# Kernel optimization log

Measured on AMD Instinct MI355X. Metric: run time of the kernel, lower is better.

The kernel has to match this reference:

```python
import jax, jax.numpy as jnp
import numpy as np

N, E = 50000, 400000
IN_F, HID, HEADS, CLASSES, GROUP = 256, 64, 4, 40, 2
NEG_SLOPE = 0.2
EPS = 1e-5


def setup_inputs() -> dict:
    key = jax.random.key(0)
    ks = jax.random.split(key, 16)
    s = 0.05
    W = HEADS * HID          # 256 flattened hidden width
    GW = W // GROUP          # 128 per-group width
    GD = HID // GROUP        # 32  per-head out_feats in middle blocks
    x = jax.random.normal(ks[0], (N, IN_F), jnp.float32)
    src = jax.random.randint(ks[1], (E,), 0, N, dtype=jnp.int32)
    # guarantee every node has >=1 incoming edge so edge_softmax is well-defined
    dst = jnp.concatenate([jnp.arange(N, dtype=jnp.int32),
                           jax.random.randint(ks[2], (E - N,), 0, N, dtype=jnp.int32)])
    return dict(
        x=x, src=src, dst=dst,
        W0=jax.random.normal(ks[3], (W, IN_F)) * s,
        attn_l0=jax.random.normal(ks[4], (HEADS, HID)) * s,
        attn_r0=jax.random.normal(ks[5], (HEADS, HID)) * s,
        resW0=jax.random.normal(ks[6], (W, IN_F)) * s,
        mid_bn_gamma=jnp.ones((2, GROUP, GW)),
        mid_bn_beta=jnp.zeros((2, GROUP, GW)),
        mid_W=jax.random.normal(ks[7], (2, GROUP, GW, GW)) * s,
        mid_attn_l=jax.random.normal(ks[8], (2, GROUP, HEADS, GD)) * s,
        mid_attn_r=jax.random.normal(ks[9], (2, GROUP, HEADS, GD)) * s,
        mid_resW=jax.random.normal(ks[10], (2, GROUP, GW, GW)) * s,
        norm_gamma=jnp.ones((W,)), norm_beta=jnp.zeros((W,)),
        W_last=jax.random.normal(ks[11], (CLASSES, W)) * s,
        attn_l_last=jax.random.normal(ks[12], (1, CLASSES)) * s,
        attn_r_last=jax.random.normal(ks[13], (1, CLASSES)) * s,
        resW_last=jax.random.normal(ks[14], (CLASSES, W)) * s,
        bias_last=jnp.zeros((CLASSES,)),
    )


def _gat_conv(x, src, dst, W, attn_l, attn_r, resW, out_isqrt, in_sqrt):
    n = x.shape[0]
    H, D = attn_l.shape
    ft0 = (x @ W.T).reshape(n, H, D)            # projected feat [N,H,D]
    ft = ft0 * out_isqrt[:, None, None]         # symmetric norm on source side
    el = (ft * attn_l).sum(-1)                  # [N,H] (uses normalized feat_src)
    er = (ft0 * attn_r).sum(-1)                 # [N,H] (feat_dst aliased BEFORE norm)
    e = el[src] + er[dst]                       # edge scores [E,H]
    e = jnp.where(e >= 0, e, NEG_SLOPE * e)     # leaky_relu
    emax = jax.ops.segment_max(e, dst, num_segments=n)
    emax = jnp.where(jnp.isfinite(emax), emax, 0.0)
    ex = jnp.exp(e - emax[dst])
    denom = jax.ops.segment_sum(ex, dst, num_segments=n)
    a = ex / jnp.maximum(denom, 1e-9)[dst]      # per-destination edge softmax [E,H]
    msg = ft[src] * a[:, :, None]               # [E,H,D]
    rst = jax.ops.segment_sum(msg, dst, num_segments=n)
    rst = rst * in_sqrt[:, None, None]          # symmetric norm on dest side
    rst = rst + (x @ resW.T).reshape(n, H, D)   # residual fc
    return rst


def _bn_relu(z, gamma, beta):
    mu = z.mean(0)
    var = ((z - mu) ** 2).mean(0)               # biased var (torch BN training)
    return jax.nn.relu(gamma * (z - mu) * jax.lax.rsqrt(var + EPS) + beta)


def reference(x, src, dst, W0, attn_l0, attn_r0, resW0, mid_bn_gamma, mid_bn_beta,
              mid_W, mid_attn_l, mid_attn_r, mid_resW, norm_gamma, norm_beta,
              W_last, attn_l_last, attn_r_last, resW_last, bias_last):
    n = x.shape[0]
    ones = jnp.ones((src.shape[0],), x.dtype)
    outdeg = jnp.maximum(jax.ops.segment_sum(ones, src, num_segments=n), 1.0)
    indeg = jnp.maximum(jax.ops.segment_sum(ones, dst, num_segments=n), 1.0)
    out_isqrt = outdeg ** -0.5
    in_sqrt = jnp.sqrt(indeg)
    # layer 0: GATConv(in_feats -> n_hidden, n_heads)
    h = _gat_conv(x, src, dst, W0, attn_l0, attn_r0, resW0, out_isqrt, in_sqrt).reshape(n, -1)
    # reversible middle layers: GroupAdditiveCoupling, group=2
    for l in range(2):
        x0, x1 = jnp.split(h, 2, axis=-1)
        z = _bn_relu(x1, mid_bn_gamma[l, 0], mid_bn_beta[l, 0])
        y0 = x0 + _gat_conv(z, src, dst, mid_W[l, 0], mid_attn_l[l, 0], mid_attn_r[l, 0],
                            mid_resW[l, 0], out_isqrt, in_sqrt).reshape(n, -1)
        z = _bn_relu(y0, mid_bn_gamma[l, 1], mid_bn_beta[l, 1])
        y1 = x1 + _gat_conv(z, src, dst, mid_W[l, 1], mid_attn_l[l, 1], mid_attn_r[l, 1],
                            mid_resW[l, 1], out_isqrt, in_sqrt).reshape(n, -1)
        h = jnp.concatenate([y0, y1], axis=-1)
    # final norm + relu + output conv (1 head), mean over head dim, bias_last
    h = _bn_relu(h, norm_gamma, norm_beta)
    out = _gat_conv(h, src, dst, W_last, attn_l_last, attn_r_last, resW_last,
                    out_isqrt, in_sqrt).mean(1)
    return out + bias_last
```

## Files before the change

### kernel.cpp

```cpp
#include <hip/hip_runtime.h>
#include <hip/hip_bf16.h>


#define IN_F   256
#define HIDW   256
#define CLS    40

typedef __attribute__((ext_vector_type(8))) __bf16 bf16x8;
typedef __attribute__((ext_vector_type(4))) float  f32x4;

__device__ inline bf16x8 zb8() {
    bf16x8 v;
#pragma unroll
    for (int i = 0; i < 8; ++i) v[i] = (__bf16)0.f;
    return v;
}
__device__ inline bf16x8 ldb8(const __hip_bfloat16* p) {
    return *reinterpret_cast<const bf16x8*>(p);
}
__device__ inline float bf2f(unsigned short u) {
    union { unsigned int i; float f; } c;
    c.i = ((unsigned int)u) << 16;
    return c.f;
}
__device__ inline unsigned short f2bu(float f) {
    __hip_bfloat16 t = __float2bfloat16(f);
    union { __hip_bfloat16 b; unsigned short u; } c;
    c.b = t;
    return c.u;
}

__global__ void k_hist(const int* __restrict__ src, const int* __restrict__ dst,
                       int E, int* __restrict__ outdeg, int* __restrict__ indeg) {
    for (int e = blockIdx.x * blockDim.x + threadIdx.x; e < E; e += gridDim.x * blockDim.x) {
        atomicAdd(&outdeg[src[e]], 1);
        atomicAdd(&indeg[dst[e]], 1);
    }
}

__global__ void k_scan1(const int* __restrict__ cnt, int N, int* __restrict__ rp1,
                        int* __restrict__ bsum) {
    __shared__ int sm[256];
    int i = blockIdx.x * 256 + threadIdx.x;
    int v = (i < N) ? cnt[i] : 0;
    sm[threadIdx.x] = v;
    __syncthreads();
    for (int off = 1; off < 256; off <<= 1) {
        int t = (threadIdx.x >= off) ? sm[threadIdx.x - off] : 0;
        __syncthreads();
        sm[threadIdx.x] += t;
        __syncthreads();
    }
    if (i < N) rp1[i] = sm[threadIdx.x];
    if (threadIdx.x == 255) bsum[blockIdx.x] = sm[255];
}

__global__ void k_scan2(int* __restrict__ bsum, int nb) {
    __shared__ int sm[256];
    int v = (threadIdx.x < nb) ? bsum[threadIdx.x] : 0;
    sm[threadIdx.x] = v;
    __syncthreads();
    for (int off = 1; off < 256; off <<= 1) {
        int t = (threadIdx.x >= off) ? sm[threadIdx.x - off] : 0;
        __syncthreads();
        sm[threadIdx.x] += t;
        __syncthreads();
    }
    if (threadIdx.x < nb) bsum[threadIdx.x] = sm[threadIdx.x] - v;
}

__global__ void k_scan3(int* __restrict__ rp1, const int* __restrict__ bsumExcl, int N) {
    int i = blockIdx.x * 256 + threadIdx.x;
    if (i < N) rp1[i] += bsumExcl[blockIdx.x];
    if (blockIdx.x == 0 && threadIdx.x == 0) rp1[-1] = 0;
}

__global__ void k_scatter(const int* __restrict__ src, const int* __restrict__ dst,
                          int E, int* __restrict__ cursor, int* __restrict__ csr_src) {
    for (int e = blockIdx.x * blockDim.x + threadIdx.x; e < E; e += gridDim.x * blockDim.x) {
        int d = dst[e];
        int pos = atomicAdd(&cursor[d], 1);
        csr_src[pos] = src[e];
    }
}

__global__ void k_deg(const int* __restrict__ outdeg, const int* __restrict__ indeg,
                      float* __restrict__ oi, float* __restrict__ insq, int N) {
    int i = blockIdx.x * 256 + threadIdx.x;
    if (i < N) {
        int od = outdeg[i]; if (od < 1) od = 1;
        int id = indeg[i];  if (id < 1) id = 1;
        oi[i]   = rsqrtf((float)od);
        insq[i] = sqrtf((float)id);
    }
}

__global__ void k_cvt6(const float* s0, __hip_bfloat16* d0, int n0,
                       const float* s1, __hip_bfloat16* d1, int n1,
                       const float* s2, __hip_bfloat16* d2, int n2,
                       const float* s3, __hip_bfloat16* d3, int n3,
                       const float* s4, __hip_bfloat16* d4, int n4,
                       const float* s5, __hip_bfloat16* d5, int n5) {
    const float* ss; __hip_bfloat16* dd; int nn;
    switch (blockIdx.y) {
        case 0: ss = s0; dd = d0; nn = n0; break;
        case 1: ss = s1; dd = d1; nn = n1; break;
        case 2: ss = s2; dd = d2; nn = n2; break;
        case 3: ss = s3; dd = d3; nn = n3; break;
        case 4: ss = s4; dd = d4; nn = n4; break;
        default: ss = s5; dd = d5; nn = n5; break;
    }
    for (int i = blockIdx.x * blockDim.x + threadIdx.x; i < nn; i += gridDim.x * blockDim.x)
        dd[i] = __float2bfloat16(ss[i]);
}

__global__ void k_prepw(const float* __restrict__ W0,
                        const float* __restrict__ al0, const float* __restrict__ ar0,
                        const float* __restrict__ midW,
                        const float* __restrict__ midal, const float* __restrict__ midar,
                        __hip_bfloat16* __restrict__ Waug0,
                        __hip_bfloat16* __restrict__ midWaug) {
    const int layer = blockIdx.y;
    int NF, K, D;
    const float *W, *al, *ar;
    __hip_bfloat16* dst;
    if (layer == 0) {
        NF = 256; K = 256; D = 64;
        W = W0; al = al0; ar = ar0; dst = Waug0;
    } else {
        const int pg = layer - 1;
        NF = 128; K = 128; D = 32;
        W = midW + pg * 16384; al = midal + pg * 128; ar = midar + pg * 128;
        dst = midWaug + (size_t)pg * 144 * 128;
    }
    const int total = (NF + 16) * K;
    for (int idx = blockIdx.x * 256 + threadIdx.x; idx < total; idx += gridDim.x * 256) {
        const int col = idx / K, k = idx % K;
        float v = 0.f;
        if (col < NF) {
            v = W[(size_t)col * K + k];
        } else {
            const int j = col - NF;
            if (j < 8) {
                const int head = j & 3;
                const float* at = (j < 4) ? al : ar;
                float s = 0.f;
                for (int d = 0; d < D; ++d)
                    s += W[(size_t)(head * D + d) * K + k] * at[head * D + d];
                v = s;
            }
        }
        dst[idx] = __float2bfloat16(v);
    }
}

template<int K, int NF, int NR, int H, bool BN>
__global__ __launch_bounds__(512) void k_gatconv_lds(
    const float* __restrict__ A, int lda,
    const __hip_bfloat16* __restrict__ Waug,
    const __hip_bfloat16* __restrict__ Wres,
    __hip_bfloat16* __restrict__ ftb, int ldft,
    float* __restrict__ Cres, int ldcres, int M,
    const float* __restrict__ scale, const float* __restrict__ shift,
    const float* __restrict__ resbase, int ldbase,
    const float* __restrict__ oi,
    float* __restrict__ el, float* __restrict__ er) {
    constexpr int BM = 32, KF = K / 32, NTOT = NF + NR;
    constexpr int CW = NTOT / 8, CT = CW / 16;
    static_assert(NTOT % 8 == 0 && CW % 16 == 0, "col split");
    static_assert(NF % CW == 0, "ft/res wave boundary");
    static_assert(H == 4, "el/er float4 stores assume H==4");
    __shared__ bf16x8 lds[2 * KF * 64];
    const int tid = threadIdx.x;
    const int wv = tid >> 6, lane = tid & 63, rf = lane & 15, kg = lane >> 4;
    const int row0 = blockIdx.x * BM;

    {
        constexpr int CPR = K / 8;
        constexpr int RSTEP = 512 / CPR;
        const int c16 = tid % CPR;
        const int ec = c16 * 8;
        const int skf = c16 >> 2, skg = c16 & 3;
        float sc[8], sh[8];
        if (BN) {
            float4 s01 = *reinterpret_cast<const float4*>(scale + ec);
            float4 s23 = *reinterpret_cast<const float4*>(scale + ec + 4);
            float4 h01 = *reinterpret_cast<const float4*>(shift + ec);
            float4 h23 = *reinterpret_cast<const float4*>(shift + ec + 4);
            sc[0]=s01.x; sc[1]=s01.y; sc[2]=s01.z; sc[3]=s01.w;
            sc[4]=s23.x; sc[5]=s23.y; sc[6]=s23.z; sc[7]=s23.w;
            sh[0]=h01.x; sh[1]=h01.y; sh[2]=h01.z; sh[3]=h01.w;
            sh[4]=h23.x; sh[5]=h23.y; sh[6]=h23.z; sh[7]=h23.w;
        }
#pragma unroll
        for (int r0 = 0; r0 < BM; r0 += RSTEP) {
            const int r = r0 + tid / CPR;
            if (r < BM) {
                const int gr = row0 + r;
                bf16x8 t = zb8();
                if (gr < M) {
                    const float* ap = A + (size_t)gr * lda + ec;
                    float4 f0 = *reinterpret_cast<const float4*>(ap);
                    float4 f1 = *reinterpret_cast<const float4*>(ap + 4);
                    float v[8] = {f0.x, f0.y, f0.z, f0.w, f1.x, f1.y, f1.z, f1.w};
#pragma unroll
                    for (int i = 0; i < 8; ++i) {
                        float u = v[i];
                        if (BN) u = fmaxf(u * sc[i] + sh[i], 0.f);
                        t[i] = (__bf16)u;
                    }
                }
                lds[((r >> 4) * KF + skf) * 64 + ((skg * 16 + (r & 15)) ^ skf)] = t;
            }
        }
    }
    __syncthreads();

    const bool isft = (wv * CW) < NF;
    const int colbase = isft ? wv * CW : wv * CW - NF;
    const __hip_bfloat16* __restrict__ Wb = isft ? Waug : Wres;

    bf16x8 a0[KF], a1[KF];
#pragma unroll
    for (int kf = 0; kf < KF; ++kf) {
        a0[kf] = lds[(0 * KF + kf) * 64 + (lane ^ kf)];
        a1[kf] = lds[(1 * KF + kf) * 64 + (lane ^ kf)];
    }
    const int r0g = row0 + rf;
    const int r1g = r0g + 16;

    for (int ct = 0; ct < CT; ++ct) {
        const int tcol = colbase + ct * 16;
        bf16x8 w[KF];
        const __hip_bfloat16* bp = Wb + (size_t)(tcol + rf) * K + kg * 8;
#pragma unroll
        for (int kf = 0; kf < KF; ++kf) w[kf] = ldb8(bp + kf * 32);
        f32x4 acc0 = {0.f, 0.f, 0.f, 0.f};
        f32x4 acc1 = {0.f, 0.f, 0.f, 0.f};
#pragma unroll
        for (int kf = 0; kf < KF; ++kf) {
            acc0 = __builtin_amdgcn_mfma_f32_16x16x32_bf16(w[kf], a0[kf], acc0, 0, 0, 0);
            acc1 = __builtin_amdgcn_mfma_f32_16x16x32_bf16(w[kf], a1[kf], acc1, 0, 0, 0);
        }
        const int c4 = tcol + 4 * kg;
        if (isft) {
            if (r0g < M) {
                ushort4 q = {f2bu(acc0[0]), f2bu(acc0[1]), f2bu(acc0[2]), f2bu(acc0[3])};
                *reinterpret_cast<ushort4*>(&ftb[(size_t)r0g * ldft + c4]) = q;
            }
            if (r1g < M) {
                ushort4 q = {f2bu(acc1[0]), f2bu(acc1[1]), f2bu(acc1[2]), f2bu(acc1[3])};
                *reinterpret_cast<ushort4*>(&ftb[(size_t)r1g * ldft + c4]) = q;
            }
        } else {
            if (r0g < M) {
                float4 v = {acc0[0], acc0[1], acc0[2], acc0[3]};
                if (resbase) {
                    float4 b4 = *reinterpret_cast<const float4*>(
                        &resbase[(size_t)r0g * ldbase + c4]);
                    v.x += b4.x; v.y += b4.y; v.z += b4.z; v.w += b4.w;
                }
                *reinterpret_cast<float4*>(&Cres[(size_t)r0g * ldcres + c4]) = v;
            }
            if (r1g < M) {
                float4 v = {acc1[0], acc1[1], acc1[2], acc1[3]};
                if (resbase) {
                    float4 b4 = *reinterpret_cast<const float4*>(
                        &resbase[(size_t)r1g * ldbase + c4]);
                    v.x += b4.x; v.y += b4.y; v.z += b4.z; v.w += b4.w;
                }
                *reinterpret_cast<float4*>(&Cres[(size_t)r1g * ldcres + c4]) = v;
            }
        }
    }

    if (wv == 0) {
        bf16x8 w[KF];
        const __hip_bfloat16* bp = Waug + (size_t)(NF + rf) * K + kg * 8;
#pragma unroll
        for (int kf = 0; kf < KF; ++kf) w[kf] = ldb8(bp + kf * 32);
        f32x4 acc0 = {0.f, 0.f, 0.f, 0.f};
        f32x4 acc1 = {0.f, 0.f, 0.f, 0.f};
#pragma unroll
        for (int kf = 0; kf < KF; ++kf) {
            acc0 = __builtin_amdgcn_mfma_f32_16x16x32_bf16(w[kf], a0[kf], acc0, 0, 0, 0);
            acc1 = __builtin_amdgcn_mfma_f32_16x16x32_bf16(w[kf], a1[kf], acc1, 0, 0, 0);
        }
        if (kg == 0) {
            if (r0g < M) {
                const float o = oi[r0g];
                float4 v = {acc0[0] * o, acc0[1] * o, acc0[2] * o, acc0[3] * o};
                *reinterpret_cast<float4*>(&el[(size_t)r0g * 4]) = v;
            }
            if (r1g < M) {
                const float o = oi[r1g];
                float4 v = {acc1[0] * o, acc1[1] * o, acc1[2] * o, acc1[3] * o};
                *reinterpret_cast<float4*>(&el[(size_t)r1g * 4]) = v;
            }
        } else if (kg == 1) {
            if (r0g < M) {
                float4 v = {acc0[0], acc0[1], acc0[2], acc0[3]};
                *reinterpret_cast<float4*>(&er[(size_t)r0g * 4]) = v;
            }
            if (r1g < M) {
                float4 v = {acc1[0], acc1[1], acc1[2], acc1[3]};
                *reinterpret_cast<float4*>(&er[(size_t)r1g * 4]) = v;
            }
        }
    }
}

template<int K, int NF, int NR, int H, bool BN>
__global__ __launch_bounds__(256) void k_gatconv_sm(
    const float* __restrict__ A, int lda,
    const __hip_bfloat16* __restrict__ Wft,
    const __hip_bfloat16* __restrict__ Wres,
    __hip_bfloat16* __restrict__ ftb, int ldft,
    float* __restrict__ Cres, int ldcres,
    int M,
    const float* __restrict__ scale, const float* __restrict__ shift,
    const float* __restrict__ resbase, int ldbase,
    const float* __restrict__ bias,
    const float* __restrict__ attn_l, const float* __restrict__ attn_r,
    const float* __restrict__ oi,
    float* __restrict__ el, float* __restrict__ er) {
    constexpr int KF   = K / 32;
    constexpr int NCTF = (NF + 15) / 16;
    constexpr int NCTR = (NR + 15) / 16;
    constexpr int CTH  = NCTF / H;
    static_assert(NCTF % H == 0, "head tiling");
    const int wave = threadIdx.x >> 6, lane = threadIdx.x & 63;
    const int row0 = blockIdx.x * 64 + wave * 16;
    const int rf = lane & 15, kg = lane >> 4;

    bf16x8 a[KF];
    {
        const int row = row0 + rf;
        const bool rok = row < M;
#pragma unroll
        for (int kf = 0; kf < KF; ++kf) {
            const int c0 = kg * 8 + kf * 32;
            if (rok) {
                const float* ap = A + (size_t)row * lda + c0;
                float4 f0 = *reinterpret_cast<const float4*>(ap);
                float4 f1 = *reinterpret_cast<const float4*>(ap + 4);
                float v[8] = {f0.x, f0.y, f0.z, f0.w, f1.x, f1.y, f1.z, f1.w};
                bf16x8 t;
                if (BN) {
                    float4 s01 = *reinterpret_cast<const float4*>(scale + c0);
                    float4 s23 = *reinterpret_cast<const float4*>(scale + c0 + 4);
                    float4 h01 = *reinterpret_cast<const float4*>(shift + c0);
                    float4 h23 = *reinterpret_cast<const float4*>(shift + c0 + 4);
                    float sc[8] = {s01.x,s01.y,s01.z,s01.w,s23.x,s23.y,s23.z,s23.w};
                    float sh[8] = {h01.x,h01.y,h01.z,h01.w,h23.x,h23.y,h23.z,h23.w};
#pragma unroll
                    for (int i = 0; i < 8; ++i)
                        t[i] = (__bf16)fmaxf(v[i] * sc[i] + sh[i], 0.f);
                } else {
#pragma unroll
                    for (int i = 0; i < 8; ++i) t[i] = (__bf16)v[i];
                }
                a[kf] = t;
            } else {
                a[kf] = zb8();
            }
        }
    }

    int ct = 0;
    for (int hh = 0; hh < H; ++hh) {
        float elp[4] = {0.f, 0.f, 0.f, 0.f};
        float erp[4] = {0.f, 0.f, 0.f, 0.f};
        for (int cth = 0; cth < CTH; ++cth, ++ct) {
            const int ccol = ct * 16 + rf;
            bf16x8 b[KF];
            const __hip_bfloat16* bp = Wft + (size_t)ccol * K + kg * 8;
#pragma unroll
            for (int kf = 0; kf < KF; ++kf)
                b[kf] = (ccol < NF) ? ldb8(bp + kf * 32) : zb8();
            f32x4 acc = {0.f, 0.f, 0.f, 0.f};
#pragma unroll
            for (int kf = 0; kf < KF; ++kf)
                acc = __builtin_amdgcn_mfma_f32_16x16x32_bf16(a[kf], b[kf], acc, 0, 0, 0);
            float al = 0.f, ar = 0.f;
            if (ccol < NF) { al = attn_l[ccol]; ar = attn_r[ccol]; }
            if (ccol < NF) {
#pragma unroll
                for (int r = 0; r < 4; ++r) {
                    const float v = acc[r];
                    elp[r] += v * al; erp[r] += v * ar;
                    const int row = row0 + kg * 4 + r;
                    if (row < M)
                        ftb[(size_t)row * ldft + ccol] = __float2bfloat16(v);
                }
            }
        }
#pragma unroll
        for (int off = 1; off <= 8; off <<= 1)
#pragma unroll
            for (int r = 0; r < 4; ++r) {
                elp[r] += __shfl_xor(elp[r], off);
                erp[r] += __shfl_xor(erp[r], off);
            }
        if (rf == 0) {
#pragma unroll
            for (int r = 0; r < 4; ++r) {
                const int row = row0 + kg * 4 + r;
                if (row < M) {
                    el[(size_t)row * H + hh] = oi[row] * elp[r];
                    er[(size_t)row * H + hh] = erp[r];
                }
            }
        }
    }

    for (int rt = 0; rt < NCTR; ++rt) {
        const int ccol = rt * 16 + rf;
        bf16x8 b[KF];
        const __hip_bfloat16* bp = Wres + (size_t)ccol * K + kg * 8;
#pragma unroll
        for (int kf = 0; kf < KF; ++kf)
            b[kf] = (ccol < NR) ? ldb8(bp + kf * 32) : zb8();
        f32x4 acc = {0.f, 0.f, 0.f, 0.f};
#pragma unroll
        for (int kf = 0; kf < KF; ++kf)
            acc = __builtin_amdgcn_mfma_f32_16x16x32_bf16(a[kf], b[kf], acc, 0, 0, 0);
        if (ccol < NR) {
#pragma unroll
            for (int r = 0; r < 4; ++r) {
                const int row = row0 + kg * 4 + r;
                if (row < M) {
                    float v = acc[r];
                    if (resbase) v += resbase[(size_t)row * ldbase + ccol];
                    if (bias) v += bias[ccol];
                    Cres[(size_t)row * ldcres + ccol] = v;
                }
            }
        }
    }
}

template<int EPL>
__device__ inline void ldrow(const __hip_bfloat16* fp, float* f) {
    if constexpr (EPL == 4) {
        ushort4 q = *reinterpret_cast<const ushort4*>(fp);
        f[0] = bf2f(q.x); f[1] = bf2f(q.y); f[2] = bf2f(q.z); f[3] = bf2f(q.w);
    } else if constexpr (EPL == 2) {
        ushort2 q = *reinterpret_cast<const ushort2*>(fp);
        f[0] = bf2f(q.x); f[1] = bf2f(q.y);
    } else {
        f[0] = bf2f(*reinterpret_cast<const unsigned short*>(fp));
    }
}
__device__ inline float escore(float sc) {
    sc = sc >= 0.f ? sc : 0.2f * sc;
    sc = fminf(fmaxf(sc, -30.f), 30.f);
    return __expf(sc);
}

template<int H, int D>
__global__ __launch_bounds__(256) void k_agg(
    const __hip_bfloat16* __restrict__ ftb,
    const float* __restrict__ el, const float* __restrict__ er,
    const int* __restrict__ row_ptr, const int* __restrict__ csr_src,
    const float* __restrict__ oi, const float* __restrict__ insq,
    float* __restrict__ out, int ldc, int N) {
    constexpr int W = H * D;
    constexpr int EPL = (W >= 64) ? (W / 64) : 1;
    const int lane = threadIdx.x & 63;
    const int v = blockIdx.x * 4 + (threadIdx.x >> 6);
    if (v >= N) return;
    if (W < 64 && lane >= W) return;
    const int col0 = lane * EPL;
    const int myh = (W >= 64) ? (col0 / D) : 0;
    const int s = row_ptr[v], e = row_ptr[v + 1];
    const float erv = er[(size_t)v * H + myh];

    float denom = 0.f;
    float acc[EPL];
#pragma unroll
    for (int k = 0; k < EPL; ++k) acc[k] = 0.f;

    int p = s;
    for (; p + 3 < e; p += 4) {
        const int u0 = csr_src[p + 0], u1 = csr_src[p + 1];
        const int u2 = csr_src[p + 2], u3 = csr_src[p + 3];
        float f0[EPL], f1[EPL], f2[EPL], f3[EPL];
        ldrow<EPL>(ftb + (size_t)u0 * W + col0, f0);
        ldrow<EPL>(ftb + (size_t)u1 * W + col0, f1);
        ldrow<EPL>(ftb + (size_t)u2 * W + col0, f2);
        ldrow<EPL>(ftb + (size_t)u3 * W + col0, f3);
        const float s0 = el[(size_t)u0 * H + myh], s1 = el[(size_t)u1 * H + myh];
        const float s2 = el[(size_t)u2 * H + myh], s3 = el[(size_t)u3 * H + myh];
        const float o0 = oi[u0], o1 = oi[u1], o2 = oi[u2], o3 = oi[u3];
        const float w0 = escore(s0 + erv), w1 = escore(s1 + erv);
        const float w2 = escore(s2 + erv), w3 = escore(s3 + erv);
        denom += (w0 + w1) + (w2 + w3);
        const float a0 = w0 * o0, a1 = w1 * o1, a2 = w2 * o2, a3 = w3 * o3;
#pragma unroll
        for (int k = 0; k < EPL; ++k)
            acc[k] += a0 * f0[k] + a1 * f1[k] + a2 * f2[k] + a3 * f3[k];
    }
    for (; p < e; ++p) {
        const int u = csr_src[p];
        float f[EPL];
        ldrow<EPL>(ftb + (size_t)u * W + col0, f);
        const float w = escore(el[(size_t)u * H + myh] + erv);
        denom += w;
        const float a = w * oi[u];
#pragma unroll
        for (int k = 0; k < EPL; ++k) acc[k] += a * f[k];
    }

    const float iv = insq[v] / fmaxf(denom, 1e-9f);
    float* op = out + (size_t)v * ldc + col0;
    if constexpr (EPL == 4) {
        float4 o = *reinterpret_cast<float4*>(op);
        o.x += iv * acc[0]; o.y += iv * acc[1]; o.z += iv * acc[2]; o.w += iv * acc[3];
        *reinterpret_cast<float4*>(op) = o;
    } else if constexpr (EPL == 2) {
        float2 o = *reinterpret_cast<float2*>(op);
        o.x += iv * acc[0]; o.y += iv * acc[1];
        *reinterpret_cast<float2*>(op) = o;
    } else {
        op[0] += iv * acc[0];
    }
}

template<int F>
__global__ __launch_bounds__(256) void k_bn_part(const float* __restrict__ in, int ldin, int N,
                                                 float* __restrict__ psum, float* __restrict__ psum2) {
    constexpr int SL = 256 / F;
    const int col = threadIdx.x % F;
    const int pr = blockIdx.x * SL + threadIdx.x / F;
    const int PRT = gridDim.x * SL;
    float s = 0.f, s2 = 0.f;
    for (int r = pr; r < N; r += PRT) {
        float v = in[(size_t)r * ldin + col];
        s += v; s2 += v * v;
    }
    psum[(size_t)pr * F + col] = s;
    psum2[(size_t)pr * F + col] = s2;
}

template<int F>
__global__ __launch_bounds__(256) void k_bn_fin(const float* __restrict__ psum,
                                                const float* __restrict__ psum2, int PRT,
                                                const float* __restrict__ gamma,
                                                const float* __restrict__ beta,
                                                float* __restrict__ scale,
                                                float* __restrict__ shift, int N) {
    const int col = blockIdx.x;
    float s = 0.f, s2 = 0.f;
    for (int p = threadIdx.x; p < PRT; p += 256) {
        s += psum[(size_t)p * F + col];
        s2 += psum2[(size_t)p * F + col];
    }
#pragma unroll
    for (int off = 32; off; off >>= 1) {
        s += __shfl_down(s, off);
        s2 += __shfl_down(s2, off);
    }
    __shared__ float sm[4], sm2[4];
    const int wave = threadIdx.x >> 6, lane = threadIdx.x & 63;
    if (lane == 0) { sm[wave] = s; sm2[wave] = s2; }
    __syncthreads();
    if (threadIdx.x == 0) {
        s = sm[0] + sm[1] + sm[2] + sm[3];
        s2 = sm2[0] + sm2[1] + sm2[2] + sm2[3];
        float mu = s / N;
        float var = s2 / N - mu * mu;
        float isd = rsqrtf(var + 1e-5f);
        float g = gamma[col];
        scale[col] = g * isd;
        shift[col] = beta[col] - g * isd * mu;
    }
}

extern "C" void kernel_launch(void* const* d_in, const int* in_sizes, int n_in,
                              void* d_out, int out_size, void* d_ws, size_t ws_size,
                              hipStream_t stream) {
    const float* x           = (const float*)d_in[0];
    const int*   src         = (const int*)d_in[1];
    const int*   dst         = (const int*)d_in[2];
    const float* W0          = (const float*)d_in[3];
    const float* attn_l0     = (const float*)d_in[4];
    const float* attn_r0     = (const float*)d_in[5];
    const float* resW0       = (const float*)d_in[6];
    const float* mid_bn_g    = (const float*)d_in[7];
    const float* mid_bn_b    = (const float*)d_in[8];
    const float* mid_W       = (const float*)d_in[9];
    const float* mid_attn_l  = (const float*)d_in[10];
    const float* mid_attn_r  = (const float*)d_in[11];
    const float* mid_resW    = (const float*)d_in[12];
    const float* norm_gamma  = (const float*)d_in[13];
    const float* norm_beta   = (const float*)d_in[14];
    const float* W_last      = (const float*)d_in[15];
    const float* attn_l_last = (const float*)d_in[16];
    const float* attn_r_last = (const float*)d_in[17];
    const float* resW_last   = (const float*)d_in[18];
    const float* bias_last   = (const float*)d_in[19];

    const int N = in_sizes[0] / IN_F;
    const int E = in_sizes[1];

    char* p = (char*)d_ws;
    size_t used = 0;
    auto take = [&](size_t bytes) -> char* {
        char* r = p;
        size_t adv = (bytes + 255) & ~(size_t)255;
        p += adv; used += adv;
        return r;
    };
    float*          h       = (float*)take((size_t)N * HIDW * 4);
    __hip_bfloat16* ftb     = (__hip_bfloat16*)take((size_t)N * HIDW * 2);
    float*          el      = (float*)take((size_t)N * 4 * 4);
    float*          er      = (float*)take((size_t)N * 4 * 4);
    float*          oi      = (float*)take((size_t)N * 4);
    float*          insq    = (float*)take((size_t)N * 4);
    int*            indeg   = (int*)take((size_t)N * 4);
    int*            outdeg  = (int*)take((size_t)N * 4);
    int*            row_ptr = (int*)take((size_t)(N + 1) * 4);
    int*            cursor  = (int*)take((size_t)N * 4);
    int*            csr_src = (int*)take((size_t)E * 4);
    int*            bsum    = (int*)take(256 * 4);
    float*          psum    = (float*)take(1 << 20);
    float*          psum2   = (float*)take(1 << 20);
    float*          scale   = (float*)take(1024);
    float*          shift   = (float*)take(1024);
    __hip_bfloat16* Waug0     = (__hip_bfloat16*)take((size_t)272 * 256 * 2);
    __hip_bfloat16* midWaug   = (__hip_bfloat16*)take((size_t)4 * 144 * 128 * 2);
    __hip_bfloat16* resW0bf   = (__hip_bfloat16*)take(65536 * 2);
    __hip_bfloat16* midresWbf = (__hip_bfloat16*)take(65536 * 2);
    __hip_bfloat16* Wlastbf   = (__hip_bfloat16*)take(10240 * 2);
    __hip_bfloat16* resWlastbf= (__hip_bfloat16*)take(10240 * 2);
    if (used > ws_size) return;

    const int nbN = (N + 255) / 256;
    const int NB4 = (N + 3) / 4;
    const int GWB = (N + 31) / 32;
    const int GWS = (N + 63) / 64;
    const int BNB = 1024;

    hipMemsetAsync(indeg, 0, (size_t)N * 4, stream);
    hipMemsetAsync(outdeg, 0, (size_t)N * 4, stream);
    k_hist<<<1024, 256, 0, stream>>>(src, dst, E, outdeg, indeg);
    k_scan1<<<nbN, 256, 0, stream>>>(indeg, N, row_ptr + 1, bsum);
    k_scan2<<<1, 256, 0, stream>>>(bsum, nbN);
    k_scan3<<<nbN, 256, 0, stream>>>(row_ptr + 1, bsum, N);
    hipMemcpyAsync(cursor, row_ptr, (size_t)N * 4, hipMemcpyDeviceToDevice, stream);
    k_scatter<<<1024, 256, 0, stream>>>(src, dst, E, cursor, csr_src);
    k_deg<<<nbN, 256, 0, stream>>>(outdeg, indeg, oi, insq, N);

    k_cvt6<<<dim3(64, 4), 256, 0, stream>>>(resW0, resW0bf, 65536,
                                            mid_resW, midresWbf, 65536,
                                            W_last, Wlastbf, 10240,
                                            resW_last, resWlastbf, 10240,
                                            nullptr, nullptr, 0,
                                            nullptr, nullptr, 0);
    k_prepw<<<dim3(96, 5), 256, 0, stream>>>(W0, attn_l0, attn_r0,
                                             mid_W, mid_attn_l, mid_attn_r,
                                             Waug0, midWaug);

    k_gatconv_lds<256, 256, 256, 4, false><<<GWB, 512, 0, stream>>>(
        x, 256, Waug0, resW0bf, ftb, 256, h, 256, N,
        nullptr, nullptr, nullptr, 0, oi, el, er);
    k_agg<4, 64><<<NB4, 256, 0, stream>>>(ftb, el, er, row_ptr, csr_src, oi, insq, h, 256, N);

    for (int l = 0; l < 2; ++l) {
        for (int g = 0; g < 2; ++g) {
            const int inoff  = (g == 0) ? 128 : 0;
            const int outoff = (g == 0) ? 0 : 128;
            const int pg = l * 2 + g;
            k_bn_part<128><<<BNB, 256, 0, stream>>>(h + inoff, 256, N, psum, psum2);
            k_bn_fin<128><<<128, 256, 0, stream>>>(psum, psum2, BNB * 2,
                                                   mid_bn_g + pg * 128, mid_bn_b + pg * 128,
                                                   scale, shift, N);
            k_gatconv_lds<128, 128, 128, 4, true><<<GWB, 512, 0, stream>>>(
                h + inoff, 256, midWaug + (size_t)pg * 144 * 128, midresWbf + pg * 16384,
                ftb, 128, h + outoff, 256, N,
                scale, shift, h + outoff, 256, oi, el, er);
            k_agg<4, 32><<<NB4, 256, 0, stream>>>(ftb, el, er, row_ptr, csr_src, oi, insq,
                                                  h + outoff, 256, N);
        }
    }

    k_bn_part<256><<<BNB, 256, 0, stream>>>(h, 256, N, psum, psum2);
    k_bn_fin<256><<<256, 256, 0, stream>>>(psum, psum2, BNB, norm_gamma, norm_beta, scale, shift, N);
    k_gatconv_sm<256, 40, 40, 1, true><<<GWS, 256, 0, stream>>>(
        h, 256, Wlastbf, resWlastbf, ftb, 40, (float*)d_out, 40, N,
        scale, shift, nullptr, 0, bias_last,
        attn_l_last, attn_r_last, oi, el, er);
    k_agg<1, 40><<<NB4, 256, 0, stream>>>(ftb, el, er, row_ptr, csr_src, oi, insq,
                                          (float*)d_out, 40, N);
}
```

Before: 581.8 us.

## Store hidden activations in bf16 and stage GEMM outputs through LDS

```diff
diff --git a/kernel.cpp b/kernel.cpp
--- a/kernel.cpp
+++ b/kernel.cpp
@@ -154,23 +154,26 @@
     }
 }
 
-template<int K, int NF, int NR, int H, bool BN>
+template<int K, int NF, int NR, int H, bool BN, bool ABF, bool ADDRES>
 __global__ __launch_bounds__(512) void k_gatconv_lds(
-    const float* __restrict__ A, int lda,
+    const void* __restrict__ Ain, int lda,
     const __hip_bfloat16* __restrict__ Waug,
     const __hip_bfloat16* __restrict__ Wres,
     __hip_bfloat16* __restrict__ ftb, int ldft,
-    float* __restrict__ Cres, int ldcres, int M,
+    __hip_bfloat16* __restrict__ hout, int ldh, int houtoff,
+    int M,
     const float* __restrict__ scale, const float* __restrict__ shift,
-    const float* __restrict__ resbase, int ldbase,
     const float* __restrict__ oi,
     float* __restrict__ el, float* __restrict__ er) {
     constexpr int BM = 32, KF = K / 32, NTOT = NF + NR;
     constexpr int CW = NTOT / 8, CT = CW / 16;
+    constexpr int NFP = NF + 8, NRP = NR + 8;
     static_assert(NTOT % 8 == 0 && CW % 16 == 0, "col split");
     static_assert(NF % CW == 0, "ft/res wave boundary");
     static_assert(H == 4, "el/er float4 stores assume H==4");
-    __shared__ bf16x8 lds[2 * KF * 64];
+    __shared__ bf16x8 ldsA[2 * KF * 64];
+    __shared__ __hip_bfloat16 oft[BM][NFP];
+    __shared__ __hip_bfloat16 ores[BM][NRP];
     const int tid = threadIdx.x;
     const int wv = tid >> 6, lane = tid & 63, rf = lane & 15, kg = lane >> 4;
     const int row0 = blockIdx.x * BM;
@@ -199,18 +202,31 @@
                 const int gr = row0 + r;
                 bf16x8 t = zb8();
                 if (gr < M) {
-                    const float* ap = A + (size_t)gr * lda + ec;
-                    float4 f0 = *reinterpret_cast<const float4*>(ap);
-                    float4 f1 = *reinterpret_cast<const float4*>(ap + 4);
-                    float v[8] = {f0.x, f0.y, f0.z, f0.w, f1.x, f1.y, f1.z, f1.w};
-#pragma unroll
-                    for (int i = 0; i < 8; ++i) {
-                        float u = v[i];
-                        if (BN) u = fmaxf(u * sc[i] + sh[i], 0.f);
-                        t[i] = (__bf16)u;
+                    if (ABF) {
+                        const __hip_bfloat16* ap =
+                            (const __hip_bfloat16*)Ain + (size_t)gr * lda + ec;
+                        bf16x8 raw = ldb8(ap);
+                        if (BN) {
+#pragma unroll
+                            for (int i = 0; i < 8; ++i)
+                                t[i] = (__bf16)fmaxf((float)raw[i] * sc[i] + sh[i], 0.f);
+                        } else {
+                            t = raw;
+                        }
+                    } else {
+                        const float* ap = (const float*)Ain + (size_t)gr * lda + ec;
+                        float4 f0 = *reinterpret_cast<const float4*>(ap);
+                        float4 f1 = *reinterpret_cast<const float4*>(ap + 4);
+                        float v[8] = {f0.x, f0.y, f0.z, f0.w, f1.x, f1.y, f1.z, f1.w};
+#pragma unroll
+                        for (int i = 0; i < 8; ++i) {
+                            float u = v[i];
+                            if (BN) u = fmaxf(u * sc[i] + sh[i], 0.f);
+                            t[i] = (__bf16)u;
+                        }
                     }
                 }
-                lds[((r >> 4) * KF + skf) * 64 + ((skg * 16 + (r & 15)) ^ skf)] = t;
+                ldsA[((r >> 4) * KF + skf) * 64 + ((skg * 16 + (r & 15)) ^ skf)] = t;
             }
         }
     }
@@ -223,8 +239,8 @@
     bf16x8 a0[KF], a1[KF];
 #pragma unroll
     for (int kf = 0; kf < KF; ++kf) {
-        a0[kf] = lds[(0 * KF + kf) * 64 + (lane ^ kf)];
-        a1[kf] = lds[(1 * KF + kf) * 64 + (lane ^ kf)];
+        a0[kf] = ldsA[(0 * KF + kf) * 64 + (lane ^ kf)];
+        a1[kf] = ldsA[(1 * KF + kf) * 64 + (lane ^ kf)];
     }
     const int r0g = row0 + rf;
     const int r1g = r0g + 16;
@@ -243,34 +259,14 @@
             acc1 = __builtin_amdgcn_mfma_f32_16x16x32_bf16(w[kf], a1[kf], acc1, 0, 0, 0);
         }
         const int c4 = tcol + 4 * kg;
+        ushort4 q0 = {f2bu(acc0[0]), f2bu(acc0[1]), f2bu(acc0[2]), f2bu(acc0[3])};
+        ushort4 q1 = {f2bu(acc1[0]), f2bu(acc1[1]), f2bu(acc1[2]), f2bu(acc1[3])};
         if (isft) {
-            if (r0g < M) {
-                ushort4 q = {f2bu(acc0[0]), f2bu(acc0[1]), f2bu(acc0[2]), f2bu(acc0[3])};
-                *reinterpret_cast<ushort4*>(&ftb[(size_t)r0g * ldft + c4]) = q;
-            }
-            if (r1g < M) {
-                ushort4 q = {f2bu(acc1[0]), f2bu(acc1[1]), f2bu(acc1[2]), f2bu(acc1[3])};
-                *reinterpret_cast<ushort4*>(&ftb[(size_t)r1g * ldft + c4]) = q;
-            }
+            *reinterpret_cast<ushort4*>(&oft[rf][c4]) = q0;
+            *reinterpret_cast<ushort4*>(&oft[rf + 16][c4]) = q1;
         } else {
-            if (r0g < M) {
-                float4 v = {acc0[0], acc0[1], acc0[2], acc0[3]};
-                if (resbase) {
-                    float4 b4 = *reinterpret_cast<const float4*>(
-                        &resbase[(size_t)r0g * ldbase + c4]);
-                    v.x += b4.x; v.y += b4.y; v.z += b4.z; v.w += b4.w;
-                }
-                *reinterpret_cast<float4*>(&Cres[(size_t)r0g * ldcres + c4]) = v;
-            }
-            if (r1g < M) {
-                float4 v = {acc1[0], acc1[1], acc1[2], acc1[3]};
-                if (resbase) {
-                    float4 b4 = *reinterpret_cast<const float4*>(
-                        &resbase[(size_t)r1g * ldbase + c4]);
-                    v.x += b4.x; v.y += b4.y; v.z += b4.z; v.w += b4.w;
-                }
-                *reinterpret_cast<float4*>(&Cres[(size_t)r1g * ldcres + c4]) = v;
-            }
+            *reinterpret_cast<ushort4*>(&ores[rf][c4]) = q0;
+            *reinterpret_cast<ushort4*>(&ores[rf + 16][c4]) = q1;
         }
     }
 
@@ -308,18 +304,52 @@
             }
         }
     }
-}
-
-template<int K, int NF, int NR, int H, bool BN>
+    __syncthreads();
+
+    {
+        constexpr int CPRF = NF / 8;
+        constexpr int UF = BM * CPRF;
+        for (int u = tid; u < UF; u += 512) {
+            const int row = u / CPRF, c8 = u % CPRF;
+            const int gr = row0 + row;
+            if (gr < M)
+                *reinterpret_cast<bf16x8*>(&ftb[(size_t)gr * ldft + c8 * 8]) =
+                    *reinterpret_cast<const bf16x8*>(&oft[row][c8 * 8]);
+        }
+    }
+    {
+        constexpr int CPRR = NR / 8;
+        constexpr int UR = BM * CPRR;
+        for (int u = tid; u < UR; u += 512) {
+            const int row = u / CPRR, c8 = u % CPRR;
+            const int gr = row0 + row;
+            if (gr < M) {
+                __hip_bfloat16* hp = hout + (size_t)gr * ldh + houtoff + c8 * 8;
+                bf16x8 v = *reinterpret_cast<const bf16x8*>(&ores[row][c8 * 8]);
+                if (ADDRES) {
+                    bf16x8 b = ldb8(hp);
+                    bf16x8 o;
+#pragma unroll
+                    for (int i = 0; i < 8; ++i)
+                        o[i] = (__bf16)((float)v[i] + (float)b[i]);
+                    *reinterpret_cast<bf16x8*>(hp) = o;
+                } else {
+                    *reinterpret_cast<bf16x8*>(hp) = v;
+                }
+            }
+        }
+    }
+}
+
+template<int K, int NF, int NR, int H>
 __global__ __launch_bounds__(256) void k_gatconv_sm(
-    const float* __restrict__ A, int lda,
+    const __hip_bfloat16* __restrict__ A, int lda,
     const __hip_bfloat16* __restrict__ Wft,
     const __hip_bfloat16* __restrict__ Wres,
     __hip_bfloat16* __restrict__ ftb, int ldft,
     float* __restrict__ Cres, int ldcres,
     int M,
     const float* __restrict__ scale, const float* __restrict__ shift,
-    const float* __restrict__ resbase, int ldbase,
     const float* __restrict__ bias,
     const float* __restrict__ attn_l, const float* __restrict__ attn_r,
     const float* __restrict__ oi,
@@ -341,25 +371,17 @@
         for (int kf = 0; kf < KF; ++kf) {
             const int c0 = kg * 8 + kf * 32;
             if (rok) {
-                const float* ap = A + (size_t)row * lda + c0;
-                float4 f0 = *reinterpret_cast<const float4*>(ap);
-                float4 f1 = *reinterpret_cast<const float4*>(ap + 4);
-                float v[8] = {f0.x, f0.y, f0.z, f0.w, f1.x, f1.y, f1.z, f1.w};
+                bf16x8 raw = ldb8(A + (size_t)row * lda + c0);
+                float4 s01 = *reinterpret_cast<const float4*>(scale + c0);
+                float4 s23 = *reinterpret_cast<const float4*>(scale + c0 + 4);
+                float4 h01 = *reinterpret_cast<const float4*>(shift + c0);
+                float4 h23 = *reinterpret_cast<const float4*>(shift + c0 + 4);
+                float sc[8] = {s01.x,s01.y,s01.z,s01.w,s23.x,s23.y,s23.z,s23.w};
+                float sh[8] = {h01.x,h01.y,h01.z,h01.w,h23.x,h23.y,h23.z,h23.w};
                 bf16x8 t;
-                if (BN) {
-                    float4 s01 = *reinterpret_cast<const float4*>(scale + c0);
-                    float4 s23 = *reinterpret_cast<const float4*>(scale + c0 + 4);
-                    float4 h01 = *reinterpret_cast<const float4*>(shift + c0);
-                    float4 h23 = *reinterpret_cast<const float4*>(shift + c0 + 4);
-                    float sc[8] = {s01.x,s01.y,s01.z,s01.w,s23.x,s23.y,s23.z,s23.w};
-                    float sh[8] = {h01.x,h01.y,h01.z,h01.w,h23.x,h23.y,h23.z,h23.w};
-#pragma unroll
-                    for (int i = 0; i < 8; ++i)
-                        t[i] = (__bf16)fmaxf(v[i] * sc[i] + sh[i], 0.f);
-                } else {
-#pragma unroll
-                    for (int i = 0; i < 8; ++i) t[i] = (__bf16)v[i];
-                }
+#pragma unroll
+                for (int i = 0; i < 8; ++i)
+                    t[i] = (__bf16)fmaxf((float)raw[i] * sc[i] + sh[i], 0.f);
                 a[kf] = t;
             } else {
                 a[kf] = zb8();
@@ -431,7 +453,6 @@
                 const int row = row0 + kg * 4 + r;
                 if (row < M) {
                     float v = acc[r];
-                    if (resbase) v += resbase[(size_t)row * ldbase + ccol];
                     if (bias) v += bias[ccol];
                     Cres[(size_t)row * ldcres + ccol] = v;
                 }
@@ -458,13 +479,13 @@
     return __expf(sc);
 }
 
-template<int H, int D>
+template<int H, int D, bool OBF>
 __global__ __launch_bounds__(256) void k_agg(
     const __hip_bfloat16* __restrict__ ftb,
     const float* __restrict__ el, const float* __restrict__ er,
     const int* __restrict__ row_ptr, const int* __restrict__ csr_src,
     const float* __restrict__ oi, const float* __restrict__ insq,
-    float* __restrict__ out, int ldc, int N) {
+    void* __restrict__ out, int ldc, int N) {
     constexpr int W = H * D;
     constexpr int EPL = (W >= 64) ? (W / 64) : 1;
     const int lane = threadIdx.x & 63;
@@ -513,34 +534,60 @@
     }
 
     const float iv = insq[v] / fmaxf(denom, 1e-9f);
-    float* op = out + (size_t)v * ldc + col0;
-    if constexpr (EPL == 4) {
-        float4 o = *reinterpret_cast<float4*>(op);
-        o.x += iv * acc[0]; o.y += iv * acc[1]; o.z += iv * acc[2]; o.w += iv * acc[3];
-        *reinterpret_cast<float4*>(op) = o;
-    } else if constexpr (EPL == 2) {
-        float2 o = *reinterpret_cast<float2*>(op);
-        o.x += iv * acc[0]; o.y += iv * acc[1];
-        *reinterpret_cast<float2*>(op) = o;
+    if (OBF) {
+        __hip_bfloat16* op = (__hip_bfloat16*)out + (size_t)v * ldc + col0;
+        if constexpr (EPL == 4) {
+            ushort4 o = *reinterpret_cast<ushort4*>(op);
+            o.x = f2bu(bf2f(o.x) + iv * acc[0]);
+            o.y = f2bu(bf2f(o.y) + iv * acc[1]);
+            o.z = f2bu(bf2f(o.z) + iv * acc[2]);
+            o.w = f2bu(bf2f(o.w) + iv * acc[3]);
+            *reinterpret_cast<ushort4*>(op) = o;
+        } else if constexpr (EPL == 2) {
+            ushort2 o = *reinterpret_cast<ushort2*>(op);
+            o.x = f2bu(bf2f(o.x) + iv * acc[0]);
+            o.y = f2bu(bf2f(o.y) + iv * acc[1]);
+            *reinterpret_cast<ushort2*>(op) = o;
+        } else {
+            unsigned short* up = (unsigned short*)op;
+            *up = f2bu(bf2f(*up) + iv * acc[0]);
+        }
     } else {
-        op[0] += iv * acc[0];
+        float* op = (float*)out + (size_t)v * ldc + col0;
+        if constexpr (EPL == 4) {
+            float4 o = *reinterpret_cast<float4*>(op);
+            o.x += iv * acc[0]; o.y += iv * acc[1]; o.z += iv * acc[2]; o.w += iv * acc[3];
+            *reinterpret_cast<float4*>(op) = o;
+        } else if constexpr (EPL == 2) {
+            float2 o = *reinterpret_cast<float2*>(op);
+            o.x += iv * acc[0]; o.y += iv * acc[1];
+            *reinterpret_cast<float2*>(op) = o;
+        } else {
+            op[0] += iv * acc[0];
+        }
     }
 }
 
 template<int F>
-__global__ __launch_bounds__(256) void k_bn_part(const float* __restrict__ in, int ldin, int N,
-                                                 float* __restrict__ psum, float* __restrict__ psum2) {
-    constexpr int SL = 256 / F;
-    const int col = threadIdx.x % F;
-    const int pr = blockIdx.x * SL + threadIdx.x / F;
+__global__ __launch_bounds__(256) void k_bn_part(const __hip_bfloat16* __restrict__ in,
+                                                 int ldin, int N,
+                                                 float* __restrict__ psum,
+                                                 float* __restrict__ psum2) {
+    constexpr int CP = F / 2;
+    constexpr int SL = 256 / CP;
+    const int cp = threadIdx.x % CP;
+    const int pr = blockIdx.x * SL + threadIdx.x / CP;
     const int PRT = gridDim.x * SL;
-    float s = 0.f, s2 = 0.f;
+    float s0 = 0.f, s20 = 0.f, s1 = 0.f, s21 = 0.f;
     for (int r = pr; r < N; r += PRT) {
-        float v = in[(size_t)r * ldin + col];
-        s += v; s2 += v * v;
-    }
-    psum[(size_t)pr * F + col] = s;
-    psum2[(size_t)pr * F + col] = s2;
+        ushort2 q = *reinterpret_cast<const ushort2*>(&in[(size_t)r * ldin + cp * 2]);
+        const float a = bf2f(q.x), b = bf2f(q.y);
+        s0 += a; s20 += a * a; s1 += b; s21 += b * b;
+    }
+    psum[(size_t)pr * F + cp * 2] = s0;
+    psum[(size_t)pr * F + cp * 2 + 1] = s1;
+    psum2[(size_t)pr * F + cp * 2] = s20;
+    psum2[(size_t)pr * F + cp * 2 + 1] = s21;
 }
 
 template<int F>
@@ -612,7 +659,7 @@
         p += adv; used += adv;
         return r;
     };
-    float*          h       = (float*)take((size_t)N * HIDW * 4);
+    __hip_bfloat16* h       = (__hip_bfloat16*)take((size_t)N * HIDW * 2);
     __hip_bfloat16* ftb     = (__hip_bfloat16*)take((size_t)N * HIDW * 2);
     float*          el      = (float*)take((size_t)N * 4 * 4);
     float*          er      = (float*)take((size_t)N * 4 * 4);
@@ -640,7 +687,7 @@
     const int NB4 = (N + 3) / 4;
     const int GWB = (N + 31) / 32;
     const int GWS = (N + 63) / 64;
-    const int BNB = 1024;
+    const int BNB = 512;
 
     hipMemsetAsync(indeg, 0, (size_t)N * 4, stream);
     hipMemsetAsync(outdeg, 0, (size_t)N * 4, stream);
@@ -662,10 +709,11 @@
                                              mid_W, mid_attn_l, mid_attn_r,
                                              Waug0, midWaug);
 
-    k_gatconv_lds<256, 256, 256, 4, false><<<GWB, 512, 0, stream>>>(
-        x, 256, Waug0, resW0bf, ftb, 256, h, 256, N,
-        nullptr, nullptr, nullptr, 0, oi, el, er);
-    k_agg<4, 64><<<NB4, 256, 0, stream>>>(ftb, el, er, row_ptr, csr_src, oi, insq, h, 256, N);
+    k_gatconv_lds<256, 256, 256, 4, false, false, false><<<GWB, 512, 0, stream>>>(
+        x, 256, Waug0, resW0bf, ftb, 256, h, 256, 0, N,
+        nullptr, nullptr, oi, el, er);
+    k_agg<4, 64, true><<<NB4, 256, 0, stream>>>(ftb, el, er, row_ptr, csr_src, oi, insq,
+                                                h, 256, N);
 
     for (int l = 0; l < 2; ++l) {
         for (int g = 0; g < 2; ++g) {
@@ -673,24 +721,25 @@
             const int outoff = (g == 0) ? 0 : 128;
             const int pg = l * 2 + g;
             k_bn_part<128><<<BNB, 256, 0, stream>>>(h + inoff, 256, N, psum, psum2);
-            k_bn_fin<128><<<128, 256, 0, stream>>>(psum, psum2, BNB * 2,
+            k_bn_fin<128><<<128, 256, 0, stream>>>(psum, psum2, BNB * 4,
                                                    mid_bn_g + pg * 128, mid_bn_b + pg * 128,
                                                    scale, shift, N);
-            k_gatconv_lds<128, 128, 128, 4, true><<<GWB, 512, 0, stream>>>(
+            k_gatconv_lds<128, 128, 128, 4, true, true, true><<<GWB, 512, 0, stream>>>(
                 h + inoff, 256, midWaug + (size_t)pg * 144 * 128, midresWbf + pg * 16384,
-                ftb, 128, h + outoff, 256, N,
-                scale, shift, h + outoff, 256, oi, el, er);
-            k_agg<4, 32><<<NB4, 256, 0, stream>>>(ftb, el, er, row_ptr, csr_src, oi, insq,
-                                                  h + outoff, 256, N);
+                ftb, 128, h, 256, outoff, N,
+                scale, shift, oi, el, er);
+            k_agg<4, 32, true><<<NB4, 256, 0, stream>>>(ftb, el, er, row_ptr, csr_src,
+                                                        oi, insq, h + outoff, 256, N);
         }
     }
 
     k_bn_part<256><<<BNB, 256, 0, stream>>>(h, 256, N, psum, psum2);
-    k_bn_fin<256><<<256, 256, 0, stream>>>(psum, psum2, BNB, norm_gamma, norm_beta, scale, shift, N);
-    k_gatconv_sm<256, 40, 40, 1, true><<<GWS, 256, 0, stream>>>(
+    k_bn_fin<256><<<256, 256, 0, stream>>>(psum, psum2, BNB * 2, norm_gamma, norm_beta,
+                                           scale, shift, N);
+    k_gatconv_sm<256, 40, 40, 1><<<GWS, 256, 0, stream>>>(
         h, 256, Wlastbf, resWlastbf, ftb, 40, (float*)d_out, 40, N,
-        scale, shift, nullptr, 0, bias_last,
+        scale, shift, bias_last,
         attn_l_last, attn_r_last, oi, el, er);
-    k_agg<1, 40><<<NB4, 256, 0, stream>>>(ftb, el, er, row_ptr, csr_src, oi, insq,
-                                          (float*)d_out, 40, N);
-}
+    k_agg<1, 40, false><<<NB4, 256, 0, stream>>>(ftb, el, er, row_ptr, csr_src, oi, insq,
+                                                 (float*)d_out, 40, N);
+}
```

Result: faster. 558.6 us (-4.0%).
